# Optimization experiments

Measured on AMD Instinct MI355X. Metric: run time of the kernel, lower is better.

The kernel has to match this reference:

```python
import math
import jax, jax.numpy as jnp
import numpy as np

H, PQ, PV = 12, 8, 12
C_S = 384
INF, EPS = 1e5, 1e-8
SOFTPLUS_INV_1 = 0.541324854612918


def _rand_rot(key, shape):
    """Random rotation matrices via normalized quaternions, shape + (3,3)."""
    q = jax.random.normal(key, shape + (4,))
    q = q / jnp.linalg.norm(q, axis=-1, keepdims=True)
    w, x, y, z = q[..., 0], q[..., 1], q[..., 2], q[..., 3]
    R = jnp.stack([
        1 - 2 * (y * y + z * z), 2 * (x * y - w * z), 2 * (x * z + w * y),
        2 * (x * y + w * z), 1 - 2 * (x * x + z * z), 2 * (y * z - w * x),
        2 * (x * z - w * y), 2 * (y * z + w * x), 1 - 2 * (x * x + y * y),
    ], axis=-1).reshape(shape + (3, 3))
    return R


def setup_inputs() -> dict:
    key = jax.random.key(0)
    ks = jax.random.split(key, 12)
    B, N1, N2 = 2, 2048, 512
    s1 = jax.random.normal(ks[0], (B, N1, C_S), dtype=jnp.float32)
    s2 = jax.random.normal(ks[1], (B, N2, C_S), dtype=jnp.float32)
    r1_rot = _rand_rot(ks[2], (B, N1)).astype(jnp.float32)
    r2_rot = _rand_rot(ks[3], (B, N2)).astype(jnp.float32)
    r1_trans = jax.random.normal(ks[4], (B, N1, 3), dtype=jnp.float32)
    r2_trans = jax.random.normal(ks[5], (B, N2, 3), dtype=jnp.float32)
    mask1 = jnp.ones((B, N1), dtype=jnp.float32)
    mask2 = jnp.ones((B, N2), dtype=jnp.float32)
    Wq = jax.random.normal(ks[6], (C_S, H * PQ * 3), dtype=jnp.float32) / math.sqrt(C_S)
    Wkv = jax.random.normal(ks[7], (C_S, H * (PQ + PV) * 3), dtype=jnp.float32) / math.sqrt(C_S)
    head_weights = jnp.full((H,), SOFTPLUS_INV_1, dtype=jnp.float32)
    Wout = jax.random.normal(ks[8], (H * PV * 4, C_S), dtype=jnp.float32) * 0.02
    bout = jnp.zeros((C_S,), dtype=jnp.float32)
    return {"s1": s1, "s2": s2, "r1_rot": r1_rot, "r1_trans": r1_trans,
            "r2_rot": r2_rot, "r2_trans": r2_trans, "mask1": mask1, "mask2": mask2,
            "Wq": Wq, "Wkv": Wkv, "head_weights": head_weights,
            "Wout": Wout, "bout": bout}


def reference(s1, s2, r1_rot, r1_trans, r2_rot, r2_trans, mask1, mask2,
              Wq, Wkv, head_weights, Wout, bout):
    B, N1, _ = s1.shape
    N2 = s2.shape[1]

    # query points: linear -> [B,N1,3,H,PQ] (torch split/stack layout) -> local [B,N1,H,PQ,3]
    q = jnp.moveaxis((s1 @ Wq).reshape(B, N1, 3, H, PQ), 2, -1)
    # rigid apply: R x + t (global frame)
    q = jnp.einsum('bimn,bihpn->bihpm', r1_rot, q) + r1_trans[:, :, None, None, :]

    kv = jnp.moveaxis((s2 @ Wkv).reshape(B, N2, 3, H, PQ + PV), 2, -1)
    kv = jnp.einsum('bjmn,bjhpn->bjhpm', r2_rot, kv) + r2_trans[:, :, None, None, :]
    k, v = kv[..., :PQ, :], kv[..., PQ:, :]  # [B,N2,H,PQ,3], [B,N2,H,PV,3]

    # sum_p ||q_p - k_p||^2 via norm expansion (avoids [B,N1,N2,H,PQ,3] tensor)
    qn = jnp.sum(q * q, axis=(-1, -2))                     # [B,N1,H]
    kn = jnp.sum(k * k, axis=(-1, -2))                     # [B,N2,H]
    cross = jnp.einsum('bihpc,bjhpc->bijh', q, k)          # [B,N1,N2,H]
    d2 = qn[:, :, None, :] + kn[:, None, :, :] - 2.0 * cross

    hw = jax.nn.softplus(head_weights) * math.sqrt(1.0 / (3 * (PQ * 9.0 / 2)))
    att = jnp.transpose(-0.5 * d2 * hw, (0, 3, 1, 2))      # [B,H,N1,N2]
    bias = INF * (mask1[:, :, None] * mask2[:, None, :] - 1.0)
    a = jax.nn.softmax(att + bias[:, None], axis=-1)

    o = jnp.einsum('bhij,bjhpc->bihpc', a, v)              # [B,N1,H,PV,3]
    # rigid invert_apply: R^T (x - t), back into local frame of residue i
    o_loc = jnp.einsum('bimn,bihpm->bihpn', r1_rot, o - r1_trans[:, :, None, None, :])

    dists = jnp.sqrt(jnp.sum(o_loc * o_loc, axis=-1) + EPS)   # [B,N1,H,PV]
    o_flat = o_loc.reshape(B, N1, H * PV, 3)
    feats = jnp.concatenate([o_flat[..., 0], o_flat[..., 1], o_flat[..., 2],
                             dists.reshape(B, N1, H * PV)], axis=-1)
    return feats @ Wout + bout
```

## Files before the change

kernel.cpp:

```cpp
#include <hip/hip_runtime.h>
#include <math.h>

#define B_ 2
#define N1_ 2048
#define N2_ 512
#define CS_ 384
#define H_ 12
#define PQ_ 8
#define PV_ 12
#define PKV_ 20
#define CQ_ (H_*PQ_*3)
#define CKV_ (H_*PKV_*3)
#define INF_ 100000.0f
#define HW_SCALE_ 0.09622504486493764f

typedef __attribute__((ext_vector_type(8))) short bf16x8;
typedef __attribute__((ext_vector_type(4))) float f32x4;

__device__ inline unsigned short f2bf(float x) {
  unsigned u = __float_as_uint(x);
  u += 0x7fffu + ((u >> 16) & 1u);
  return (unsigned short)(u >> 16);
}

__device__ inline bf16x8 cvt8(const float* __restrict__ p) {
  float4 a = *(const float4*)p;
  float4 b = *(const float4*)(p + 4);
  bf16x8 r;
  r[0] = (short)f2bf(a.x); r[1] = (short)f2bf(a.y);
  r[2] = (short)f2bf(a.z); r[3] = (short)f2bf(a.w);
  r[4] = (short)f2bf(b.x); r[5] = (short)f2bf(b.y);
  r[6] = (short)f2bf(b.z); r[7] = (short)f2bf(b.w);
  return r;
}

#define TQ_   108
#define TKV_  276
#define TWO_  216
#define VPAD_ 72
#define KN_   12
__global__ __launch_bounds__(256) void prep_kernel(
    const float* __restrict__ Wq, const float* __restrict__ Wkv,
    const float* __restrict__ Wout,
    unsigned short* __restrict__ wqT, unsigned short* __restrict__ wkvT,
    unsigned short* __restrict__ woutT,
    unsigned short* __restrict__ vtb, float* __restrict__ kn)
{
  __shared__ float lds[32][33];
  int blk = blockIdx.x, t = threadIdx.x;
  int rr0 = t >> 5, cc = t & 31;

  const float* src = nullptr; unsigned short* dst = nullptr;
  int K = 0, N = 0, k0 = 0, n0 = 0;
  if (blk < TQ_) {
    src = Wq; dst = wqT; K = 384; N = CQ_;
    k0 = (blk % 12) * 32; n0 = (blk / 12) * 32;
  } else if (blk < TQ_ + TKV_) {
    int b2 = blk - TQ_;
    src = Wkv; dst = wkvT; K = 384; N = CKV_;
    k0 = (b2 % 12) * 32; n0 = (b2 / 12) * 32;
  } else if (blk < TQ_ + TKV_ + TWO_) {
    int b3 = blk - TQ_ - TKV_;
    src = Wout; dst = woutT; K = 576; N = CS_;
    k0 = (b3 % 18) * 32; n0 = (b3 / 18) * 32;
  } else if (blk < TQ_ + TKV_ + TWO_ + VPAD_) {
    int idx = (blk - TQ_ - TKV_ - TWO_)*256 + t;
    int f = idx * 8;
    int run = f >> 9, off = f & 511;
    int bh = run / 12, cc2 = 36 + run % 12;
    uint4 z = {0u,0u,0u,0u};
    *(uint4*)(vtb + ((size_t)bh*48 + cc2)*512 + off) = z;
    return;
  } else {
    int idx = (blk - TQ_ - TKV_ - TWO_ - VPAD_)*256 + t;
    float4 z = {0.f,0.f,0.f,0.f};
    *(float4*)(kn + (size_t)idx*4) = z;
    return;
  }

  #pragma unroll
  for (int rr = 0; rr < 4; ++rr) {
    int r = rr0 + rr*8;
    if (n0 + cc < N) lds[r][cc] = src[(size_t)(k0 + r)*N + n0 + cc];
  }
  __syncthreads();
  #pragma unroll
  for (int rr = 0; rr < 4; ++rr) {
    int r = rr0 + rr*8;
    if (n0 + r < N) dst[(size_t)(n0 + r)*K + k0 + cc] = f2bf(lds[cc][r]);
  }
}

__global__ __launch_bounds__(256) void proj_mfma(
    const float* __restrict__ s1, const float* __restrict__ s2,
    const unsigned short* __restrict__ wqT, const unsigned short* __restrict__ wkvT,
    const float* __restrict__ r1_rot, const float* __restrict__ r1_trans,
    const float* __restrict__ r2_rot, const float* __restrict__ r2_trans,
    unsigned short* __restrict__ qgb, float* __restrict__ qn,
    unsigned short* __restrict__ kgb, unsigned short* __restrict__ vtb,
    float* __restrict__ kn)
{
  int wave = threadIdx.x >> 6, lane = threadIdx.x & 63;
  int col = lane & 15, g = lane >> 4;

  if (blockIdx.x < 384) {
    int wg = blockIdx.x*4 + wave;
    int strip = wg / 6;
    int nt = wg % 6;
    int i0 = strip * 16;

    f32x4 ax = {0.f,0.f,0.f,0.f}, ay = ax, az = ax;
    const float* arow = s1 + (size_t)(i0 + col)*CS_;
    const unsigned short* bx = wqT + (size_t)((nt     )*16 + col)*CS_;
    const unsigned short* by = wqT + (size_t)((nt +  6)*16 + col)*CS_;
    const unsigned short* bz = wqT + (size_t)((nt + 12)*16 + col)*CS_;
    #pragma unroll
    for (int k = 0; k < CS_; k += 32) {
      bf16x8 a = cvt8(arow + k + g*8);
      ax = __builtin_amdgcn_mfma_f32_16x16x32_bf16(a, *(const bf16x8*)(bx + k + g*8), ax, 0,0,0);
      ay = __builtin_amdgcn_mfma_f32_16x16x32_bf16(a, *(const bf16x8*)(by + k + g*8), ay, 0,0,0);
      az = __builtin_amdgcn_mfma_f32_16x16x32_bf16(a, *(const bf16x8*)(bz + k + g*8), az, 0,0,0);
    }

    int p = nt*16 + col;
    int h = p >> 3, pq = p & 7;
    float qsum[4];
    #pragma unroll
    for (int r = 0; r < 4; ++r) {
      int row = i0 + g*4 + r;
      const float* R  = r1_rot   + (size_t)row*9;
      const float* tr = r1_trans + (size_t)row*3;
      float x = ax[r], y = ay[r], z = az[r];
      float g0 = R[0]*x + R[1]*y + R[2]*z + tr[0];
      float g1 = R[3]*x + R[4]*y + R[5]*z + tr[1];
      float g2 = R[6]*x + R[7]*y + R[8]*z + tr[2];
      int b = row >> 11, i = row & (N1_-1);
      size_t rbase = ((size_t)(b*H_ + h)*N1_ + i)*32;
      qgb[rbase + pq*3]     = f2bf(g0);
      qgb[rbase + pq*3 + 1] = f2bf(g1);
      qgb[rbase + pq*3 + 2] = f2bf(g2);
      if (pq == 7) {
        uint4 z4 = {0u,0u,0u,0u};
        *(uint4*)(qgb + rbase + 24) = z4;
      }
      qsum[r] = g0*g0 + g1*g1 + g2*g2;
    }
    #pragma unroll
    for (int r = 0; r < 4; ++r) {
      qsum[r] += __shfl_xor(qsum[r], 1);
      qsum[r] += __shfl_xor(qsum[r], 2);
      qsum[r] += __shfl_xor(qsum[r], 4);
    }
    if ((col & 7) == 0) {
      int hh = nt*2 + (col >> 3);
      #pragma unroll
      for (int r = 0; r < 4; ++r) {
        int row = i0 + g*4 + r;
        int b = row >> 11, i = row & (N1_-1);
        qn[(size_t)(b*H_ + hh)*N1_ + i] = qsum[r];
      }
    }
  } else {
    int wg = (blockIdx.x - 384)*4 + wave;
    int strip = wg / 15;
    int nt = wg % 15;
    int row0 = strip * 16;

    f32x4 ax = {0.f,0.f,0.f,0.f}, ay = ax, az = ax;
    const float* arow = s2 + (size_t)(row0 + col)*CS_;
    const unsigned short* bx = wkvT + (size_t)(nt*16       + col)*CS_;
    const unsigned short* by = wkvT + (size_t)(nt*16 + 240 + col)*CS_;
    const unsigned short* bz = wkvT + (size_t)(nt*16 + 480 + col)*CS_;
    #pragma unroll
    for (int k = 0; k < CS_; k += 32) {
      bf16x8 a = cvt8(arow + k + g*8);
      ax = __builtin_amdgcn_mfma_f32_16x16x32_bf16(a, *(const bf16x8*)(bx + k + g*8), ax, 0,0,0);
      ay = __builtin_amdgcn_mfma_f32_16x16x32_bf16(a, *(const bf16x8*)(by + k + g*8), ay, 0,0,0);
      az = __builtin_amdgcn_mfma_f32_16x16x32_bf16(a, *(const bf16x8*)(bz + k + g*8), az, 0,0,0);
    }

    int p = nt*16 + col;
    int h = p / PKV_, pp = p % PKV_;
    #pragma unroll
    for (int r = 0; r < 4; ++r) {
      int row = row0 + g*4 + r;
      const float* R  = r2_rot   + (size_t)row*9;
      const float* tr = r2_trans + (size_t)row*3;
      float x = ax[r], y = ay[r], z = az[r];
      float g0 = R[0]*x + R[1]*y + R[2]*z + tr[0];
      float g1 = R[3]*x + R[4]*y + R[5]*z + tr[1];
      float g2 = R[6]*x + R[7]*y + R[8]*z + tr[2];
      int b = row >> 9, j = row & (N2_-1);
      int bh = b*H_ + h;
      if (pp < PQ_) {
        size_t base = ((size_t)bh*N2_ + j)*32 + pp*3;
        kgb[base]   = f2bf(g0);
        kgb[base+1] = f2bf(g1);
        kgb[base+2] = f2bf(g2);
        if (pp == 0) {
          uint4 z4 = {0u,0u,0u,0u};
          *(uint4*)(kgb + ((size_t)bh*N2_ + j)*32 + 24) = z4;
        }
        atomicAdd(&kn[(size_t)bh*N2_ + j], g0*g0 + g1*g1 + g2*g2);
      } else {
        int comp = (pp - PQ_)*3;
        size_t base = ((size_t)bh*48 + comp)*512 + j;
        vtb[base]        = f2bf(g0);
        vtb[base + 512]  = f2bf(g1);
        vtb[base + 1024] = f2bf(g2);
      }
    }
  }
}

#define RSTRIDE 72
#define OSTRIDE 52
__global__ __launch_bounds__(256) void attn_kernel(
    const unsigned short* __restrict__ qgb, const float* __restrict__ qn,
    const unsigned short* __restrict__ kgb, const unsigned short* __restrict__ vtb,
    const float* __restrict__ kn, const float* __restrict__ mask1,
    const float* __restrict__ mask2, const float* __restrict__ hwts,
    const float* __restrict__ rot, const float* __restrict__ trans,
    unsigned short* __restrict__ featsb)
{
  __shared__ __align__(16) unsigned short pstrip[4][16][RSTRIDE];
  __shared__ float o_s[4][16][OSTRIDE];
  __shared__ float l_s[4][16];

  int wave = threadIdx.x >> 6;
  int lane = threadIdx.x & 63;
  int col = lane & 15, g = lane >> 4;
  int pair = wave >> 1, half = wave & 1;
  int mt = blockIdx.x*2 + pair;
  int bh = mt >> 7;
  int it = mt & 127;
  int b = bh / H_, h = bh - b*H_;

  float hw = logf(1.0f + __expf(hwts[h])) * HW_SCALE_;

  bf16x8 qa = *(const bf16x8*)(qgb + (((size_t)bh*N1_ + it*16 + col)*32 + g*8));

  float ar[4], m1r[4];
  #pragma unroll
  for (int r = 0; r < 4; ++r) {
    int ig = it*16 + g*4 + r;
    ar[r]  = fmaf(-0.5f*hw, qn[(size_t)bh*N1_ + ig], -INF_);
    m1r[r] = mask1[b*N1_ + ig] * INF_;
  }

  f32x4 ot[3];
  #pragma unroll
  for (int m = 0; m < 3; ++m) ot[m] = (f32x4){0.f,0.f,0.f,0.f};
  float l[4] = {0.f,0.f,0.f,0.f};

  const unsigned short* kbase = kgb + (size_t)bh*N2_*32;
  const unsigned short* vbase = vtb + (size_t)bh*48*512;
  const float* knp = kn + (size_t)bh*N2_;
  const float* m2p = mask2 + b*N2_;

  for (int jt = half*4; jt < half*4 + 4; ++jt) {
    int j0 = jt*64;
    #pragma unroll
    for (int nt = 0; nt < 4; ++nt) {
      int jg = j0 + nt*16 + col;
      bf16x8 kb = *(const bf16x8*)(kbase + ((size_t)jg*32 + g*8));
      f32x4 dotv = __builtin_amdgcn_mfma_f32_16x16x32_bf16(
          qa, kb, (f32x4){0.f,0.f,0.f,0.f}, 0, 0, 0);
      float bc  = -0.5f*hw*knp[jg];
      float m2c = m2p[jg];
      #pragma unroll
      for (int r = 0; r < 4; ++r) {
        float logit = fmaf(hw, dotv[r], fmaf(m1r[r], m2c, ar[r] + bc));
        float w = __expf(logit);
        l[r] += w;
        pstrip[wave][g*4 + r][nt*16 + col] = f2bf(w);
      }
    }
    #pragma unroll
    for (int ks = 0; ks < 2; ++ks) {
      bf16x8 pb = *(const bf16x8*)&pstrip[wave][col][ks*32 + g*8];
      #pragma unroll
      for (int mtv = 0; mtv < 3; ++mtv) {
        bf16x8 va = *(const bf16x8*)(vbase +
            ((size_t)(mtv*16 + col))*512 + j0 + ks*32 + g*8);
        ot[mtv] = __builtin_amdgcn_mfma_f32_16x16x32_bf16(va, pb, ot[mtv], 0, 0, 0);
      }
    }
  }

  #pragma unroll
  for (int r = 0; r < 4; ++r) {
    l[r] += __shfl_xor(l[r], 1);
    l[r] += __shfl_xor(l[r], 2);
    l[r] += __shfl_xor(l[r], 4);
    l[r] += __shfl_xor(l[r], 8);
  }
  if (col == 0) {
    #pragma unroll
    for (int r = 0; r < 4; ++r) l_s[wave][g*4 + r] = l[r];
  }
  #pragma unroll
  for (int mtv = 0; mtv < 3; ++mtv)
    #pragma unroll
    for (int r = 0; r < 4; ++r)
      o_s[wave][col][mtv*16 + g*4 + r] = ot[mtv][r];
  __syncthreads();
  if (half) return;

  float inv = 1.0f / (l_s[wave][col] + l_s[wave+1][col]);
  int ig = it*16 + col;
  int row = b*N1_ + ig;
  const float* R  = rot   + (size_t)row*9;
  const float* tr = trans + (size_t)row*3;
  float R00=R[0],R01=R[1],R02=R[2],R10=R[3],R11=R[4],R12=R[5],R20=R[6],R21=R[7],R22=R[8];
  float t0=tr[0], t1=tr[1], t2=tr[2];
  unsigned short* fb = featsb + (size_t)row*576 + h*PV_;
  #pragma unroll
  for (int p = 0; p < 3; ++p) {
    int pt = g*3 + p;
    float ox = (o_s[wave][col][pt*3+0] + o_s[wave+1][col][pt*3+0])*inv - t0;
    float oy = (o_s[wave][col][pt*3+1] + o_s[wave+1][col][pt*3+1])*inv - t1;
    float oz = (o_s[wave][col][pt*3+2] + o_s[wave+1][col][pt*3+2])*inv - t2;
    float lx = R00*ox + R10*oy + R20*oz;
    float ly = R01*ox + R11*oy + R21*oz;
    float lz = R02*ox + R12*oy + R22*oz;
    float dist = sqrtf(lx*lx + ly*ly + lz*lz + 1e-8f);
    fb[pt]       = f2bf(lx);
    fb[144 + pt] = f2bf(ly);
    fb[288 + pt] = f2bf(lz);
    fb[432 + pt] = f2bf(dist);
  }
}

__global__ __launch_bounds__(1024) void outproj_mfma(
    const unsigned short* __restrict__ featsb, const unsigned short* __restrict__ woutT,
    const float* __restrict__ bout, float* __restrict__ out)
{
  __shared__ float acc_s[8][16][48];
  int wave = threadIdx.x >> 6, lane = threadIdx.x & 63;
  int col = lane & 15, g = lane >> 4;
  int nw = wave & 7, kh = wave >> 3;
  int i0 = blockIdx.x * 16;
  int n0 = nw * 48;

  f32x4 acc[3];
  #pragma unroll
  for (int m = 0; m < 3; ++m) acc[m] = (f32x4){0.f,0.f,0.f,0.f};
  const unsigned short* arow = featsb + (size_t)(i0 + col)*576 + kh*288;
  const unsigned short* b0 = woutT + (size_t)(n0      + col)*576 + kh*288;
  const unsigned short* b1 = woutT + (size_t)(n0 + 16 + col)*576 + kh*288;
  const unsigned short* b2 = woutT + (size_t)(n0 + 32 + col)*576 + kh*288;
  #pragma unroll 3
  for (int k = 0; k < 288; k += 32) {
    bf16x8 a = *(const bf16x8*)(arow + k + g*8);
    acc[0] = __builtin_amdgcn_mfma_f32_16x16x32_bf16(a, *(const bf16x8*)(b0 + k + g*8), acc[0], 0,0,0);
    acc[1] = __builtin_amdgcn_mfma_f32_16x16x32_bf16(a, *(const bf16x8*)(b1 + k + g*8), acc[1], 0,0,0);
    acc[2] = __builtin_amdgcn_mfma_f32_16x16x32_bf16(a, *(const bf16x8*)(b2 + k + g*8), acc[2], 0,0,0);
  }
  if (kh) {
    #pragma unroll
    for (int t3 = 0; t3 < 3; ++t3)
      #pragma unroll
      for (int r = 0; r < 4; ++r)
        acc_s[nw][g*4 + r][t3*16 + col] = acc[t3][r];
  }
  __syncthreads();
  if (kh) return;
  #pragma unroll
  for (int t3 = 0; t3 < 3; ++t3) {
    int n = n0 + t3*16 + col;
    float bb = bout[n];
    #pragma unroll
    for (int r = 0; r < 4; ++r) {
      int row = i0 + g*4 + r;
      out[(size_t)row*CS_ + n] = acc[t3][r] + acc_s[nw][g*4 + r][t3*16 + col] + bb;
    }
  }
}

extern "C" void kernel_launch(void* const* d_in, const int* in_sizes, int n_in,
                              void* d_out, int out_size, void* d_ws, size_t ws_size,
                              hipStream_t stream) {
  const float* s1       = (const float*)d_in[0];
  const float* s2       = (const float*)d_in[1];
  const float* r1_rot   = (const float*)d_in[2];
  const float* r1_trans = (const float*)d_in[3];
  const float* r2_rot   = (const float*)d_in[4];
  const float* r2_trans = (const float*)d_in[5];
  const float* mask1    = (const float*)d_in[6];
  const float* mask2    = (const float*)d_in[7];
  const float* Wq       = (const float*)d_in[8];
  const float* Wkv      = (const float*)d_in[9];
  const float* hwts     = (const float*)d_in[10];
  const float* Wout     = (const float*)d_in[11];
  const float* bout     = (const float*)d_in[12];
  float* out = (float*)d_out;

  float* qn = (float*)d_ws;
  float* kn = qn + (size_t)B_*H_*N1_;
  unsigned short* featsb = (unsigned short*)(kn + (size_t)B_*H_*N2_);
  unsigned short* qgb  = featsb + (size_t)B_*N1_*576;
  unsigned short* kgb  = qgb  + (size_t)B_*H_*N1_*32;
  unsigned short* vtb  = kgb  + (size_t)B_*H_*N2_*32;
  unsigned short* wqT  = vtb  + (size_t)B_*H_*48*512;
  unsigned short* wkvT = wqT  + (size_t)CQ_*CS_;
  unsigned short* woutT= wkvT + (size_t)CKV_*CS_;

  prep_kernel<<<TQ_+TKV_+TWO_+VPAD_+KN_, 256, 0, stream>>>(
      Wq, Wkv, Wout, wqT, wkvT, woutT, vtb, kn);
  proj_mfma<<<624, 256, 0, stream>>>(s1, s2, wqT, wkvT, r1_rot, r1_trans,
                                     r2_rot, r2_trans, qgb, qn, kgb, vtb, kn);
  attn_kernel<<<B_*H_*(N1_/32), 256, 0, stream>>>(qgb, qn, kgb, vtb, kn, mask1, mask2,
                                                  hwts, r1_rot, r1_trans, featsb);
  outproj_mfma<<<256, 1024, 0, stream>>>(featsb, woutT, bout, out);
}
```

Measured before the change: 158.8 us.

## Fuse attention with output projection, pre-convert activations to bf16, use exp2

The attention kernel now assigns one 16-row query tile per block, with 12 waves covering all heads. It writes the point features into shared memory and runs the output projection in place, which removes the featsb round-trip and the separate outproj launch. The prep kernel also converts s1 and s2 to bf16 up front, so the projection GEMMs no longer convert float operands repeatedly across column tiles. The softmax moves to exp2 with log2e folded into the scaling constants. The costs are an extra bf16 copy of the activations, 768-thread blocks with larger shared memory and lower occupancy, and each block re-reading the full Wout for only 16 rows.

```diff
diff --git a/kernel.cpp b/kernel.cpp
--- a/kernel.cpp
+++ b/kernel.cpp
@@ -13,6 +13,7 @@
 #define CKV_ (H_*PKV_*3)
 #define INF_ 100000.0f
 #define HW_SCALE_ 0.09622504486493764f
+#define LOG2E_ 1.4426950408889634f
 
 typedef __attribute__((ext_vector_type(8))) short bf16x8;
 typedef __attribute__((ext_vector_type(4))) float f32x4;
@@ -39,12 +40,17 @@
 #define TWO_  216
 #define VPAD_ 72
 #define KN_   12
+#define S1B_  768
+#define S2B_  192
+#define PREP_GRID_ (TQ_+TKV_+TWO_+VPAD_+KN_+S1B_+S2B_)
 __global__ __launch_bounds__(256) void prep_kernel(
     const float* __restrict__ Wq, const float* __restrict__ Wkv,
     const float* __restrict__ Wout,
+    const float* __restrict__ s1, const float* __restrict__ s2,
     unsigned short* __restrict__ wqT, unsigned short* __restrict__ wkvT,
     unsigned short* __restrict__ woutT,
-    unsigned short* __restrict__ vtb, float* __restrict__ kn)
+    unsigned short* __restrict__ vtb, float* __restrict__ kn,
+    unsigned short* __restrict__ s1b, unsigned short* __restrict__ s2b)
 {
   __shared__ float lds[32][33];
   int blk = blockIdx.x, t = threadIdx.x;
@@ -71,11 +77,19 @@
     uint4 z = {0u,0u,0u,0u};
     *(uint4*)(vtb + ((size_t)bh*48 + cc2)*512 + off) = z;
     return;
-  } else {
+  } else if (blk < TQ_ + TKV_ + TWO_ + VPAD_ + KN_) {
     int idx = (blk - TQ_ - TKV_ - TWO_ - VPAD_)*256 + t;
     float4 z = {0.f,0.f,0.f,0.f};
     *(float4*)(kn + (size_t)idx*4) = z;
     return;
+  } else if (blk < TQ_ + TKV_ + TWO_ + VPAD_ + KN_ + S1B_) {
+    size_t idx = (size_t)(blk - TQ_ - TKV_ - TWO_ - VPAD_ - KN_)*256 + t;
+    *(bf16x8*)(s1b + idx*8) = cvt8(s1 + idx*8);
+    return;
+  } else {
+    size_t idx = (size_t)(blk - TQ_ - TKV_ - TWO_ - VPAD_ - KN_ - S1B_)*256 + t;
+    *(bf16x8*)(s2b + idx*8) = cvt8(s2 + idx*8);
+    return;
   }
 
   #pragma unroll
@@ -92,7 +106,7 @@
 }
 
 __global__ __launch_bounds__(256) void proj_mfma(
-    const float* __restrict__ s1, const float* __restrict__ s2,
+    const unsigned short* __restrict__ s1b, const unsigned short* __restrict__ s2b,
     const unsigned short* __restrict__ wqT, const unsigned short* __restrict__ wkvT,
     const float* __restrict__ r1_rot, const float* __restrict__ r1_trans,
     const float* __restrict__ r2_rot, const float* __restrict__ r2_trans,
@@ -110,13 +124,13 @@
     int i0 = strip * 16;
 
     f32x4 ax = {0.f,0.f,0.f,0.f}, ay = ax, az = ax;
-    const float* arow = s1 + (size_t)(i0 + col)*CS_;
+    const unsigned short* arow = s1b + (size_t)(i0 + col)*CS_;
     const unsigned short* bx = wqT + (size_t)((nt     )*16 + col)*CS_;
     const unsigned short* by = wqT + (size_t)((nt +  6)*16 + col)*CS_;
     const unsigned short* bz = wqT + (size_t)((nt + 12)*16 + col)*CS_;
     #pragma unroll
     for (int k = 0; k < CS_; k += 32) {
-      bf16x8 a = cvt8(arow + k + g*8);
+      bf16x8 a = *(const bf16x8*)(arow + k + g*8);
       ax = __builtin_amdgcn_mfma_f32_16x16x32_bf16(a, *(const bf16x8*)(bx + k + g*8), ax, 0,0,0);
       ay = __builtin_amdgcn_mfma_f32_16x16x32_bf16(a, *(const bf16x8*)(by + k + g*8), ay, 0,0,0);
       az = __builtin_amdgcn_mfma_f32_16x16x32_bf16(a, *(const bf16x8*)(bz + k + g*8), az, 0,0,0);
@@ -167,13 +181,13 @@
     int row0 = strip * 16;
 
     f32x4 ax = {0.f,0.f,0.f,0.f}, ay = ax, az = ax;
-    const float* arow = s2 + (size_t)(row0 + col)*CS_;
+    const unsigned short* arow = s2b + (size_t)(row0 + col)*CS_;
     const unsigned short* bx = wkvT + (size_t)(nt*16       + col)*CS_;
     const unsigned short* by = wkvT + (size_t)(nt*16 + 240 + col)*CS_;
     const unsigned short* bz = wkvT + (size_t)(nt*16 + 480 + col)*CS_;
     #pragma unroll
     for (int k = 0; k < CS_; k += 32) {
-      bf16x8 a = cvt8(arow + k + g*8);
+      bf16x8 a = *(const bf16x8*)(arow + k + g*8);
       ax = __builtin_amdgcn_mfma_f32_16x16x32_bf16(a, *(const bf16x8*)(bx + k + g*8), ax, 0,0,0);
       ay = __builtin_amdgcn_mfma_f32_16x16x32_bf16(a, *(const bf16x8*)(by + k + g*8), ay, 0,0,0);
       az = __builtin_amdgcn_mfma_f32_16x16x32_bf16(a, *(const bf16x8*)(bz + k + g*8), az, 0,0,0);
@@ -214,38 +228,45 @@
 }
 
 #define RSTRIDE 72
-#define OSTRIDE 52
-__global__ __launch_bounds__(256) void attn_kernel(
+#define OSTRIDE 51
+#define WSLOT 3328
+#define FSTRIDE 584
+__global__ __launch_bounds__(768) void attn_fused(
     const unsigned short* __restrict__ qgb, const float* __restrict__ qn,
     const unsigned short* __restrict__ kgb, const unsigned short* __restrict__ vtb,
     const float* __restrict__ kn, const float* __restrict__ mask1,
     const float* __restrict__ mask2, const float* __restrict__ hwts,
     const float* __restrict__ rot, const float* __restrict__ trans,
-    unsigned short* __restrict__ featsb)
+    const unsigned short* __restrict__ woutT, const float* __restrict__ bout,
+    float* __restrict__ out)
 {
-  __shared__ __align__(16) unsigned short pstrip[4][16][RSTRIDE];
-  __shared__ float o_s[4][16][OSTRIDE];
-  __shared__ float l_s[4][16];
+  __shared__ __align__(16) unsigned char ovl[12*WSLOT];
+  __shared__ __align__(16) unsigned short feats_s[16][FSTRIDE];
+  __shared__ float l_s[12][16];
 
   int wave = threadIdx.x >> 6;
   int lane = threadIdx.x & 63;
   int col = lane & 15, g = lane >> 4;
-  int pair = wave >> 1, half = wave & 1;
-  int mt = blockIdx.x*2 + pair;
-  int bh = mt >> 7;
-  int it = mt & 127;
-  int b = bh / H_, h = bh - b*H_;
-
-  float hw = logf(1.0f + __expf(hwts[h])) * HW_SCALE_;
+  int b = blockIdx.x >> 7;
+  int it = blockIdx.x & 127;
+  int h = wave;
+  int bh = b*H_ + h;
+
+  unsigned short* ps = (unsigned short*)(ovl + wave*WSLOT);
+  float*          os = (float*)(ovl + wave*WSLOT);
+
+  float hw   = logf(1.0f + __expf(hwts[h])) * HW_SCALE_;
+  float hwl  = hw * LOG2E_;
+  float mneg = -INF_ * LOG2E_;
 
   bf16x8 qa = *(const bf16x8*)(qgb + (((size_t)bh*N1_ + it*16 + col)*32 + g*8));
 
-  float ar[4], m1r[4];
+  float ar[4], m1l[4];
   #pragma unroll
   for (int r = 0; r < 4; ++r) {
     int ig = it*16 + g*4 + r;
-    ar[r]  = fmaf(-0.5f*hw, qn[(size_t)bh*N1_ + ig], -INF_);
-    m1r[r] = mask1[b*N1_ + ig] * INF_;
+    ar[r]  = -0.5f*hwl * qn[(size_t)bh*N1_ + ig];
+    m1l[r] = mask1[b*N1_ + ig] * (INF_*LOG2E_);
   }
 
   f32x4 ot[3];
@@ -258,7 +279,7 @@
   const float* knp = kn + (size_t)bh*N2_;
   const float* m2p = mask2 + b*N2_;
 
-  for (int jt = half*4; jt < half*4 + 4; ++jt) {
+  for (int jt = 0; jt < 8; ++jt) {
     int j0 = jt*64;
     #pragma unroll
     for (int nt = 0; nt < 4; ++nt) {
@@ -266,19 +287,19 @@
       bf16x8 kb = *(const bf16x8*)(kbase + ((size_t)jg*32 + g*8));
       f32x4 dotv = __builtin_amdgcn_mfma_f32_16x16x32_bf16(
           qa, kb, (f32x4){0.f,0.f,0.f,0.f}, 0, 0, 0);
-      float bc  = -0.5f*hw*knp[jg];
+      float bc  = -0.5f*hwl*knp[jg];
       float m2c = m2p[jg];
       #pragma unroll
       for (int r = 0; r < 4; ++r) {
-        float logit = fmaf(hw, dotv[r], fmaf(m1r[r], m2c, ar[r] + bc));
-        float w = __expf(logit);
+        float logit = fmaf(hwl, dotv[r], fmaf(m1l[r], m2c, mneg) + (ar[r] + bc));
+        float w = __builtin_amdgcn_exp2f(logit);
         l[r] += w;
-        pstrip[wave][g*4 + r][nt*16 + col] = f2bf(w);
+        ps[(g*4 + r)*RSTRIDE + nt*16 + col] = f2bf(w);
       }
     }
     #pragma unroll
     for (int ks = 0; ks < 2; ++ks) {
-      bf16x8 pb = *(const bf16x8*)&pstrip[wave][col][ks*32 + g*8];
+      bf16x8 pb = *(const bf16x8*)&ps[col*RSTRIDE + ks*32 + g*8];
       #pragma unroll
       for (int mtv = 0; mtv < 3; ++mtv) {
         bf16x8 va = *(const bf16x8*)(vbase +
@@ -295,6 +316,7 @@
     l[r] += __shfl_xor(l[r], 4);
     l[r] += __shfl_xor(l[r], 8);
   }
+  __builtin_amdgcn_sched_barrier(0);
   if (col == 0) {
     #pragma unroll
     for (int r = 0; r < 4; ++r) l_s[wave][g*4 + r] = l[r];
@@ -303,77 +325,55 @@
   for (int mtv = 0; mtv < 3; ++mtv)
     #pragma unroll
     for (int r = 0; r < 4; ++r)
-      o_s[wave][col][mtv*16 + g*4 + r] = ot[mtv][r];
+      os[col*OSTRIDE + mtv*16 + g*4 + r] = ot[mtv][r];
   __syncthreads();
-  if (half) return;
-
-  float inv = 1.0f / (l_s[wave][col] + l_s[wave+1][col]);
-  int ig = it*16 + col;
-  int row = b*N1_ + ig;
-  const float* R  = rot   + (size_t)row*9;
-  const float* tr = trans + (size_t)row*3;
-  float R00=R[0],R01=R[1],R02=R[2],R10=R[3],R11=R[4],R12=R[5],R20=R[6],R21=R[7],R22=R[8];
-  float t0=tr[0], t1=tr[1], t2=tr[2];
-  unsigned short* fb = featsb + (size_t)row*576 + h*PV_;
-  #pragma unroll
-  for (int p = 0; p < 3; ++p) {
-    int pt = g*3 + p;
-    float ox = (o_s[wave][col][pt*3+0] + o_s[wave+1][col][pt*3+0])*inv - t0;
-    float oy = (o_s[wave][col][pt*3+1] + o_s[wave+1][col][pt*3+1])*inv - t1;
-    float oz = (o_s[wave][col][pt*3+2] + o_s[wave+1][col][pt*3+2])*inv - t2;
-    float lx = R00*ox + R10*oy + R20*oz;
-    float ly = R01*ox + R11*oy + R21*oz;
-    float lz = R02*ox + R12*oy + R22*oz;
-    float dist = sqrtf(lx*lx + ly*ly + lz*lz + 1e-8f);
-    fb[pt]       = f2bf(lx);
-    fb[144 + pt] = f2bf(ly);
-    fb[288 + pt] = f2bf(lz);
-    fb[432 + pt] = f2bf(dist);
-  }
-}
-
-__global__ __launch_bounds__(1024) void outproj_mfma(
-    const unsigned short* __restrict__ featsb, const unsigned short* __restrict__ woutT,
-    const float* __restrict__ bout, float* __restrict__ out)
-{
-  __shared__ float acc_s[8][16][48];
-  int wave = threadIdx.x >> 6, lane = threadIdx.x & 63;
-  int col = lane & 15, g = lane >> 4;
-  int nw = wave & 7, kh = wave >> 3;
-  int i0 = blockIdx.x * 16;
-  int n0 = nw * 48;
-
-  f32x4 acc[3];
-  #pragma unroll
-  for (int m = 0; m < 3; ++m) acc[m] = (f32x4){0.f,0.f,0.f,0.f};
-  const unsigned short* arow = featsb + (size_t)(i0 + col)*576 + kh*288;
-  const unsigned short* b0 = woutT + (size_t)(n0      + col)*576 + kh*288;
-  const unsigned short* b1 = woutT + (size_t)(n0 + 16 + col)*576 + kh*288;
-  const unsigned short* b2 = woutT + (size_t)(n0 + 32 + col)*576 + kh*288;
-  #pragma unroll 3
-  for (int k = 0; k < 288; k += 32) {
-    bf16x8 a = *(const bf16x8*)(arow + k + g*8);
-    acc[0] = __builtin_amdgcn_mfma_f32_16x16x32_bf16(a, *(const bf16x8*)(b0 + k + g*8), acc[0], 0,0,0);
-    acc[1] = __builtin_amdgcn_mfma_f32_16x16x32_bf16(a, *(const bf16x8*)(b1 + k + g*8), acc[1], 0,0,0);
-    acc[2] = __builtin_amdgcn_mfma_f32_16x16x32_bf16(a, *(const bf16x8*)(b2 + k + g*8), acc[2], 0,0,0);
-  }
-  if (kh) {
-    #pragma unroll
-    for (int t3 = 0; t3 < 3; ++t3)
-      #pragma unroll
-      for (int r = 0; r < 4; ++r)
-        acc_s[nw][g*4 + r][t3*16 + col] = acc[t3][r];
+
+  {
+    float inv = 1.0f / l_s[wave][col];
+    int ig = it*16 + col;
+    int row = b*N1_ + ig;
+    const float* R  = rot   + (size_t)row*9;
+    const float* tr = trans + (size_t)row*3;
+    float R00=R[0],R01=R[1],R02=R[2],R10=R[3],R11=R[4],R12=R[5],R20=R[6],R21=R[7],R22=R[8];
+    float t0=tr[0], t1=tr[1], t2=tr[2];
+    int h12 = h*PV_;
+    #pragma unroll
+    for (int p = 0; p < 3; ++p) {
+      int pt = g*3 + p;
+      float ox = os[col*OSTRIDE + pt*3+0]*inv - t0;
+      float oy = os[col*OSTRIDE + pt*3+1]*inv - t1;
+      float oz = os[col*OSTRIDE + pt*3+2]*inv - t2;
+      float lx = R00*ox + R10*oy + R20*oz;
+      float ly = R01*ox + R11*oy + R21*oz;
+      float lz = R02*ox + R12*oy + R22*oz;
+      float dist = sqrtf(lx*lx + ly*ly + lz*lz + 1e-8f);
+      feats_s[col][      h12 + pt] = f2bf(lx);
+      feats_s[col][144 + h12 + pt] = f2bf(ly);
+      feats_s[col][288 + h12 + pt] = f2bf(lz);
+      feats_s[col][432 + h12 + pt] = f2bf(dist);
+    }
   }
   __syncthreads();
-  if (kh) return;
-  #pragma unroll
-  for (int t3 = 0; t3 < 3; ++t3) {
-    int n = n0 + t3*16 + col;
-    float bb = bout[n];
+
+  {
+    int n0 = wave * 32;
+    f32x4 acc0 = {0.f,0.f,0.f,0.f}, acc1 = acc0;
+    const unsigned short* b0 = woutT + (size_t)(n0      + col)*576;
+    const unsigned short* b1 = woutT + (size_t)(n0 + 16 + col)*576;
+    #pragma unroll 3
+    for (int k = 0; k < 576; k += 32) {
+      bf16x8 a = *(const bf16x8*)&feats_s[col][k + g*8];
+      acc0 = __builtin_amdgcn_mfma_f32_16x16x32_bf16(a, *(const bf16x8*)(b0 + k + g*8), acc0, 0,0,0);
+      acc1 = __builtin_amdgcn_mfma_f32_16x16x32_bf16(a, *(const bf16x8*)(b1 + k + g*8), acc1, 0,0,0);
+    }
+    int rowbase = b*N1_ + it*16;
+    float bb0 = bout[n0 + col];
+    float bb1 = bout[n0 + 16 + col];
     #pragma unroll
     for (int r = 0; r < 4; ++r) {
-      int row = i0 + g*4 + r;
-      out[(size_t)row*CS_ + n] = acc[t3][r] + acc_s[nw][g*4 + r][t3*16 + col] + bb;
+      size_t orow = (size_t)(rowbase + g*4 + r)*CS_;
+      out[orow + n0 + col]      = acc0[r] + bb0;
+      out[orow + n0 + 16 + col] = acc1[r] + bb1;
     }
   }
 }
@@ -398,19 +398,19 @@
 
   float* qn = (float*)d_ws;
   float* kn = qn + (size_t)B_*H_*N1_;
-  unsigned short* featsb = (unsigned short*)(kn + (size_t)B_*H_*N2_);
-  unsigned short* qgb  = featsb + (size_t)B_*N1_*576;
+  unsigned short* qgb  = (unsigned short*)(kn + (size_t)B_*H_*N2_);
   unsigned short* kgb  = qgb  + (size_t)B_*H_*N1_*32;
   unsigned short* vtb  = kgb  + (size_t)B_*H_*N2_*32;
   unsigned short* wqT  = vtb  + (size_t)B_*H_*48*512;
   unsigned short* wkvT = wqT  + (size_t)CQ_*CS_;
   unsigned short* woutT= wkvT + (size_t)CKV_*CS_;
-
-  prep_kernel<<<TQ_+TKV_+TWO_+VPAD_+KN_, 256, 0, stream>>>(
-      Wq, Wkv, Wout, wqT, wkvT, woutT, vtb, kn);
-  proj_mfma<<<624, 256, 0, stream>>>(s1, s2, wqT, wkvT, r1_rot, r1_trans,
+  unsigned short* s1b  = woutT+ (size_t)CS_*576;
+  unsigned short* s2b  = s1b  + (size_t)B_*N1_*CS_;
+
+  prep_kernel<<<PREP_GRID_, 256, 0, stream>>>(
+      Wq, Wkv, Wout, s1, s2, wqT, wkvT, woutT, vtb, kn, s1b, s2b);
+  proj_mfma<<<624, 256, 0, stream>>>(s1b, s2b, wqT, wkvT, r1_rot, r1_trans,
                                      r2_rot, r2_trans, qgb, qn, kgb, vtb, kn);
-  attn_kernel<<<B_*H_*(N1_/32), 256, 0, stream>>>(qgb, qn, kgb, vtb, kn, mask1, mask2,
-                                                  hwts, r1_rot, r1_trans, featsb);
-  outproj_mfma<<<256, 1024, 0, stream>>>(featsb, woutT, bout, out);
-}
+  attn_fused<<<B_*(N1_/16), 768, 0, stream>>>(qgb, qn, kgb, vtb, kn, mask1, mask2,
+                                              hwts, r1_rot, r1_trans, woutT, bout, out);
+}
```

New measurement: 148.6 us. -6.5%, faster.
